# Performance work log

Measured on AMD Instinct MI355X. Metric: run time of the kernel, lower is better.

## Reference

```python
import jax, jax.numpy as jnp
import numpy as np

GATE_DIM = 1313 + 622  # hardcoded in the module
D1 = 300
D2 = 300
OUT = 300


def setup_inputs() -> dict:
    key = jax.random.key(0)
    ks = jax.random.split(key, 12)
    N, M = 384, 384
    inp = {
        "feature1": jax.random.normal(ks[0], (N, GATE_DIM), jnp.float32),
        "box1": jax.random.uniform(ks[1], (N, 5), jnp.float32),
        "feature2": jax.random.normal(ks[2], (M, GATE_DIM), jnp.float32),
        "box2": jax.random.uniform(ks[3], (M, 5), jnp.float32),
        "attrlabel_embeddings": jax.random.normal(ks[4], (GATE_DIM, D1), jnp.float32) * 0.05,
        # learned parameters
        "gate1": 10.0 * jnp.ones((GATE_DIM,), jnp.float32),
        "gate2": 10.0 * jnp.ones((GATE_DIM,), jnp.float32),
        "weight_loc": jnp.zeros((2,), jnp.float32),
        "fc1_w": jax.random.normal(ks[5], (OUT, D1 + D2), jnp.float32) * (1.0 / np.sqrt(D1 + D2)),
        "fc1_b": jnp.zeros((OUT,), jnp.float32),
        "fc2_w": jax.random.normal(ks[6], (OUT, 10), jnp.float32) * (1.0 / np.sqrt(10.0)),
        "fc2_b": jnp.zeros((OUT,), jnp.float32),
        "fc3_w": jax.random.normal(ks[7], (OUT, OUT), jnp.float32) * (1.0 / np.sqrt(OUT)),
        "fc3_b": jnp.zeros((OUT,), jnp.float32),
    }
    return inp


def _preprocess(feature, box):
    # repo's preprocess callable; modeled as identity on the feature
    # (feature already has dim input_dim1/input_dim2 expected by fc1)
    return feature


def reference(feature1, box1, feature2, box2, attrlabel_embeddings,
              gate1, gate2, weight_loc,
              fc1_w, fc1_b, fc2_w, fc2_b, fc3_w, fc3_b):
    # gated feature -> attrlabel embedding projection
    f1 = (feature1 * jax.nn.sigmoid(gate1)) @ attrlabel_embeddings  # [N, D1]
    f1 = _preprocess(f1, box1)
    f2 = (feature2 * jax.nn.sigmoid(gate2)) @ attrlabel_embeddings  # [M, D2]
    f2 = _preprocess(f2, box2)

    # fc1(cat(meshgrid(f1,f2))) == f1@W_a^T (broadcast over M) + f2@W_b^T (broadcast over N) + b
    Wa, Wb = fc1_w[:, :f1.shape[-1]], fc1_w[:, f1.shape[-1]:]
    semantic = jax.nn.relu(
        jnp.einsum('nd,od->no', f1, Wa)[:, None, :]
        + jnp.einsum('md,od->mo', f2, Wb)[None, :, :]
        + fc1_b
    )  # [N, M, OUT]

    Wa2, Wb2 = fc2_w[:, :5], fc2_w[:, 5:]
    spatial = jax.nn.relu(
        jnp.einsum('nd,od->no', box1, Wa2)[:, None, :]
        + jnp.einsum('md,od->mo', box2, Wb2)[None, :, :]
        + fc2_b
    )  # [N, M, OUT]

    w = jax.nn.softmax(weight_loc)
    mixed = w[0] * semantic + w[1] * spatial
    embedding = jnp.einsum('nmo,po->nmp', mixed, fc3_w) + fc3_b  # [N, M, OUT]
    return embedding
```

## Files before the change

kernel.cpp:

```cpp
#include <hip/hip_runtime.h>
#include <hip/hip_bf16.h>

#define NROW 384
#define GD   1935
#define GK   1952
#define DD   300
#define KP   320
#define DP   304

#define OFF_SIG1 0
#define OFF_SIG2 2048
#define OFF_W    4096
#define OFF_XBF  4112
#define OFF_EBT  753680
#define OFF_FC1B 1066000
#define OFF_FC3B 1168400
#define OFF_F1B  1217040
#define OFF_AB   1339920
#define OFF_CD   1585680

typedef short short8 __attribute__((ext_vector_type(8)));
typedef float floatx4 __attribute__((ext_vector_type(4)));

__device__ inline unsigned short f2bf(float x){
  union { float f; unsigned u; } v; v.f = x;
  unsigned r = v.u + 0x7fffu + ((v.u >> 16) & 1u);
  return (unsigned short)(r >> 16);
}

__global__ void k_prep(const float* g1, const float* g2, const float* wloc, float* ws){
  int t = blockIdx.x * 256 + threadIdx.x;
  if (t < GD) ws[OFF_SIG1 + t] = 1.f / (1.f + expf(-g1[t]));
  else if (t < 2*GD) ws[OFF_SIG2 + t - GD] = 1.f / (1.f + expf(-g2[t - GD]));
  else if (t == 2*GD){
    float a = wloc[0], b = wloc[1];
    float m = fmaxf(a, b);
    float ea = expf(a - m), eb = expf(b - m);
    ws[OFF_W + 0] = ea / (ea + eb);
    ws[OFF_W + 1] = eb / (ea + eb);
  }
}

#define NX  (2*384*GK)
#define NE  (KP*GK)
#define NF1 (2*KP*KP)
#define NF3 (DP*KP)
__global__ void k_cvt_all(const float* f1, const float* f2, const float* E,
                          const float* fc1w, const float* fc3w, float* ws){
  int t = blockIdx.x * 256 + threadIdx.x;
  unsigned short* xbf  = (unsigned short*)(ws + OFF_XBF);
  unsigned short* ebt  = (unsigned short*)(ws + OFF_EBT);
  unsigned short* f1b  = (unsigned short*)(ws + OFF_FC1B);
  unsigned short* f3b  = (unsigned short*)(ws + OFF_FC3B);
  if (t < NX){
    int z = t / (384*GK); int r = t - z*384*GK;
    int n = r / GK, k = r - n*GK;
    const float* X   = z ? f2 : f1;
    const float* sig = ws + (z ? OFF_SIG2 : OFF_SIG1);
    float v = (k < GD) ? X[n*GD + k] * sig[k] : 0.f;
    xbf[t] = f2bf(v);
  } else if (t < NX + NE){
    int r = t - NX;
    int c = r / GK, k = r - c*GK;
    float v = (k < GD && c < DD) ? E[k*DD + c] : 0.f;
    ebt[r] = f2bf(v);
  } else if (t < NX + NE + NF1){
    int r = t - NX - NE;
    int z = r / (KP*KP); int r2 = r - z*KP*KP;
    int o = r2 / KP, d = r2 - o*KP;
    float v = (o < DD && d < DD) ? fc1w[o*(2*DD) + z*DD + d] : 0.f;
    f1b[r] = f2bf(v);
  } else {
    int r = t - NX - NE - NF1;
    int p = r / KP, k = r - p*KP;
    float v = (p < DD && k < DD) ? fc3w[p*DD + k] : 0.f;
    f3b[r] = f2bf(v);
  }
}

__global__ __launch_bounds__(256) void k_gg(float* ws){
  int z = blockIdx.y;
  const unsigned short* X   = (const unsigned short*)(ws + OFF_XBF) + z*384*GK;
  const unsigned short* Ebt = (const unsigned short*)(ws + OFF_EBT);
  unsigned short* out       = (unsigned short*)(ws + OFF_F1B) + z*384*KP;
  int t = threadIdx.x, lane = t & 63;
  int id = blockIdx.x * 4 + (t >> 6);
  int mt = id / 20, ct = id - mt*20;
  int col = lane & 15, quad = lane >> 4;
  const unsigned short* ap = X   + (mt*16 + col)*GK + quad*8;
  const unsigned short* bp = Ebt + (ct*16 + col)*GK + quad*8;
  floatx4 acc = (floatx4){0.f,0.f,0.f,0.f};
  for (int kc = 0; kc < 61; ++kc){
    short8 a = *(const short8*)(ap + kc*32);
    short8 b = *(const short8*)(bp + kc*32);
    acc = __builtin_amdgcn_mfma_f32_16x16x32_bf16(a, b, acc, 0, 0, 0);
  }
  int c = ct*16 + col;
  #pragma unroll
  for (int r = 0; r < 4; ++r){
    int m = mt*16 + quad*4 + r;
    out[m*KP + c] = (c < DD) ? f2bf(acc[r]) : (unsigned short)0;
  }
}

__global__ __launch_bounds__(256) void k_sem(const float* fc1b, float* ws){
  int z = blockIdx.y;
  const unsigned short* F = (const unsigned short*)(ws + OFF_F1B) + z*384*KP;
  const unsigned short* W = (const unsigned short*)(ws + OFF_FC1B) + z*KP*KP;
  float* out = ws + OFF_AB + z*384*KP;
  float w0 = ws[OFF_W];
  int t = threadIdx.x, lane = t & 63;
  int id = blockIdx.x * 4 + (t >> 6);
  int rt = id / 20, ot = id - rt*20;
  int col = lane & 15, quad = lane >> 4;
  const unsigned short* ap = F + (rt*16 + col)*KP + quad*8;
  const unsigned short* bp = W + (ot*16 + col)*KP + quad*8;
  floatx4 acc = (floatx4){0.f,0.f,0.f,0.f};
  #pragma unroll
  for (int kc = 0; kc < 10; ++kc){
    short8 a = *(const short8*)(ap + kc*32);
    short8 b = *(const short8*)(bp + kc*32);
    acc = __builtin_amdgcn_mfma_f32_16x16x32_bf16(a, b, acc, 0, 0, 0);
  }
  int o = ot*16 + col;
  float bias = (z == 0 && o < DD) ? fc1b[o] : 0.f;
  #pragma unroll
  for (int r = 0; r < 4; ++r){
    int rr = rt*16 + quad*4 + r;
    out[rr*KP + o] = (o < DD) ? w0 * (acc[r] + bias) : 0.f;
  }
}

__global__ void k_spa(const float* box1, const float* box2, const float* fc2w,
                      const float* fc2b, float* ws){
  int z = blockIdx.y;
  const float* bx = z ? box2 : box1;
  float* out = ws + OFF_CD + z*384*KP;
  int joff = z ? 5 : 0;
  float w1 = ws[OFF_W + 1];
  int t = blockIdx.x * 256 + threadIdx.x;
  int r = t / KP, o = t - r*KP;
  float v = 0.f;
  if (o < DD){
    const float* b = bx + r * 5;
    const float* wr = fc2w + o * 10 + joff;
    v = b[0]*wr[0] + b[1]*wr[1] + b[2]*wr[2] + b[3]*wr[3] + b[4]*wr[4];
    if (!z) v += fc2b[o];
    v *= w1;
  }
  out[t] = v;
}

__global__ __launch_bounds__(512, 4) void k_main(const float* fc3b, float* out, const float* ws){
  __shared__ __align__(16) unsigned short smix[512 * 8];
  __shared__ __align__(16) unsigned short swt[1216 * 8];
  const unsigned short* fc3bf = (const unsigned short*)(ws + OFF_FC3B);
  int t = threadIdx.x;
  int lane = t & 63, wave = t >> 6;
  int col = lane & 15, quad = lane >> 4;
  int mt0 = blockIdx.x * 128;
  int n = blockIdx.y;
  const float* Ah = ws + OFF_AB + n * KP;
  const float* Bh = ws + OFF_AB + 384 * KP;
  const float* Ch = ws + OFF_CD + n * KP;
  const float* Dh = ws + OFF_CD + 384 * KP;

  floatx4 acc[19];
  #pragma unroll
  for (int i = 0; i < 19; ++i) acc[i] = (floatx4){0.f,0.f,0.f,0.f};

  int w_b  = t >> 6;
  int j    = (t >> 4) & 3;
  int colb = t & 15;
  int mg = mt0 + w_b*16 + colb;
  const float* pB = Bh + (size_t)mg * KP;
  const float* pD = Dh + (size_t)mg * KP;

  for (int kc = 0; kc < 10; ++kc){
    int kb = kc*32 + j*8;
    {
      union { unsigned short s[8]; uint4 v; } u;
      float4 a0 = *(const float4*)(Ah + kb);
      float4 c0 = *(const float4*)(Ch + kb);
      float4 b0 = *(const float4*)(pB + kb);
      float4 d0 = *(const float4*)(pD + kb);
      u.s[0] = f2bf(fmaxf(a0.x + b0.x, 0.f) + fmaxf(c0.x + d0.x, 0.f));
      u.s[1] = f2bf(fmaxf(a0.y + b0.y, 0.f) + fmaxf(c0.y + d0.y, 0.f));
      u.s[2] = f2bf(fmaxf(a0.z + b0.z, 0.f) + fmaxf(c0.z + d0.z, 0.f));
      u.s[3] = f2bf(fmaxf(a0.w + b0.w, 0.f) + fmaxf(c0.w + d0.w, 0.f));
      float4 a1 = *(const float4*)(Ah + kb + 4);
      float4 c1 = *(const float4*)(Ch + kb + 4);
      float4 b1 = *(const float4*)(pB + kb + 4);
      float4 d1 = *(const float4*)(pD + kb + 4);
      u.s[4] = f2bf(fmaxf(a1.x + b1.x, 0.f) + fmaxf(c1.x + d1.x, 0.f));
      u.s[5] = f2bf(fmaxf(a1.y + b1.y, 0.f) + fmaxf(c1.y + d1.y, 0.f));
      u.s[6] = f2bf(fmaxf(a1.z + b1.z, 0.f) + fmaxf(c1.z + d1.z, 0.f));
      u.s[7] = f2bf(fmaxf(a1.w + b1.w, 0.f) + fmaxf(c1.w + d1.w, 0.f));
      *(uint4*)&smix[t * 8] = u.v;
    }
    for (int s = t; s < 1216; s += 512){
      int pt = s >> 6, l = s & 63;
      int cc = l & 15, qq = l >> 4;
      uint4 w = *(const uint4*)(fc3bf + (pt*16 + cc)*KP + kc*32 + qq*8);
      *(uint4*)&swt[s * 8] = w;
    }
    __syncthreads();
    short8 af = *(const short8*)&smix[(wave*64 + lane) * 8];
    #pragma unroll
    for (int pt = 0; pt < 19; ++pt){
      short8 bf = *(const short8*)&swt[(pt*64 + lane) * 8];
      acc[pt] = __builtin_amdgcn_mfma_f32_16x16x32_bf16(af, bf, acc[pt], 0, 0, 0);
    }
    __syncthreads();
  }

  #pragma unroll
  for (int pt = 0; pt < 19; ++pt){
    int p = pt*16 + col;
    if (p < DD){
      float bias = fc3b[p];
      #pragma unroll
      for (int r = 0; r < 4; ++r){
        int m = mt0 + wave*16 + quad*4 + r;
        out[((size_t)n * NROW + m) * DD + p] = acc[pt][r] + bias;
      }
    }
  }
}

extern "C" void kernel_launch(void* const* d_in, const int* in_sizes, int n_in,
                              void* d_out, int out_size, void* d_ws, size_t ws_size,
                              hipStream_t stream) {
  const float* feature1 = (const float*)d_in[0];
  const float* box1     = (const float*)d_in[1];
  const float* feature2 = (const float*)d_in[2];
  const float* box2     = (const float*)d_in[3];
  const float* E        = (const float*)d_in[4];
  const float* gate1    = (const float*)d_in[5];
  const float* gate2    = (const float*)d_in[6];
  const float* wloc     = (const float*)d_in[7];
  const float* fc1w     = (const float*)d_in[8];
  const float* fc1b     = (const float*)d_in[9];
  const float* fc2w     = (const float*)d_in[10];
  const float* fc2b     = (const float*)d_in[11];
  const float* fc3w     = (const float*)d_in[12];
  const float* fc3b     = (const float*)d_in[13];
  float* out = (float*)d_out;
  float* ws  = (float*)d_ws;

  hipLaunchKernelGGL(k_prep, dim3(16), dim3(256), 0, stream, gate1, gate2, wloc, ws);
  hipLaunchKernelGGL(k_cvt_all, dim3((NX+NE+NF1+NF3)/256), dim3(256), 0, stream,
                     feature1, feature2, E, fc1w, fc3w, ws);
  hipLaunchKernelGGL(k_gg, dim3(120, 2), dim3(256), 0, stream, ws);
  hipLaunchKernelGGL(k_sem, dim3(120, 2), dim3(256), 0, stream, fc1b, ws);
  hipLaunchKernelGGL(k_spa, dim3(480, 2), dim3(256), 0, stream,
                     box1, box2, fc2w, fc2b, ws);
  hipLaunchKernelGGL(k_main, dim3(3, NROW), dim3(512), 0, stream, fc3b, out, ws);
}
```

Before: 335.7 us.

## Drop LDS staging in main GEMM; load MFMA fragments directly from global

The main fused mix+fc3 kernel no longer stages the mixed activations and fc3 weights through shared memory with two barriers per k-chunk. Each wave now computes its own A fragment in registers and reads the B fragments for all 19 output tiles straight from global memory (L2/L1-resident bf16 weights). Block size drops from 512 to 256 threads and the grid doubles. This removes the LDS traffic and synchronisation, but every wave now issues its own global weight loads, with far less reuse per block and more cache pressure.

```diff
diff --git a/kernel.cpp b/kernel.cpp
--- a/kernel.cpp
+++ b/kernel.cpp
@@ -151,67 +151,53 @@
   out[t] = v;
 }
 
-__global__ __launch_bounds__(512, 4) void k_main(const float* fc3b, float* out, const float* ws){
-  __shared__ __align__(16) unsigned short smix[512 * 8];
-  __shared__ __align__(16) unsigned short swt[1216 * 8];
+__global__ __launch_bounds__(256, 3) void k_main(const float* fc3b, float* out, const float* ws){
   const unsigned short* fc3bf = (const unsigned short*)(ws + OFF_FC3B);
   int t = threadIdx.x;
   int lane = t & 63, wave = t >> 6;
   int col = lane & 15, quad = lane >> 4;
-  int mt0 = blockIdx.x * 128;
   int n = blockIdx.y;
+  int mrow0 = blockIdx.x * 64 + wave * 16;
   const float* Ah = ws + OFF_AB + n * KP;
   const float* Bh = ws + OFF_AB + 384 * KP;
   const float* Ch = ws + OFF_CD + n * KP;
   const float* Dh = ws + OFF_CD + 384 * KP;
 
-  floatx4 acc[19];
-  #pragma unroll
-  for (int i = 0; i < 19; ++i) acc[i] = (floatx4){0.f,0.f,0.f,0.f};
-
-  int w_b  = t >> 6;
-  int j    = (t >> 4) & 3;
-  int colb = t & 15;
-  int mg = mt0 + w_b*16 + colb;
+  int mg = mrow0 + col;
   const float* pB = Bh + (size_t)mg * KP;
   const float* pD = Dh + (size_t)mg * KP;
+  const unsigned short* wbase = fc3bf + col * KP + quad * 8;
+
+  floatx4 acc[19];
+  #pragma unroll
+  for (int i = 0; i < 19; ++i) acc[i] = (floatx4){0.f,0.f,0.f,0.f};
 
   for (int kc = 0; kc < 10; ++kc){
-    int kb = kc*32 + j*8;
-    {
-      union { unsigned short s[8]; uint4 v; } u;
-      float4 a0 = *(const float4*)(Ah + kb);
-      float4 c0 = *(const float4*)(Ch + kb);
-      float4 b0 = *(const float4*)(pB + kb);
-      float4 d0 = *(const float4*)(pD + kb);
-      u.s[0] = f2bf(fmaxf(a0.x + b0.x, 0.f) + fmaxf(c0.x + d0.x, 0.f));
-      u.s[1] = f2bf(fmaxf(a0.y + b0.y, 0.f) + fmaxf(c0.y + d0.y, 0.f));
-      u.s[2] = f2bf(fmaxf(a0.z + b0.z, 0.f) + fmaxf(c0.z + d0.z, 0.f));
-      u.s[3] = f2bf(fmaxf(a0.w + b0.w, 0.f) + fmaxf(c0.w + d0.w, 0.f));
-      float4 a1 = *(const float4*)(Ah + kb + 4);
-      float4 c1 = *(const float4*)(Ch + kb + 4);
-      float4 b1 = *(const float4*)(pB + kb + 4);
-      float4 d1 = *(const float4*)(pD + kb + 4);
-      u.s[4] = f2bf(fmaxf(a1.x + b1.x, 0.f) + fmaxf(c1.x + d1.x, 0.f));
-      u.s[5] = f2bf(fmaxf(a1.y + b1.y, 0.f) + fmaxf(c1.y + d1.y, 0.f));
-      u.s[6] = f2bf(fmaxf(a1.z + b1.z, 0.f) + fmaxf(c1.z + d1.z, 0.f));
-      u.s[7] = f2bf(fmaxf(a1.w + b1.w, 0.f) + fmaxf(c1.w + d1.w, 0.f));
-      *(uint4*)&smix[t * 8] = u.v;
-    }
-    for (int s = t; s < 1216; s += 512){
-      int pt = s >> 6, l = s & 63;
-      int cc = l & 15, qq = l >> 4;
-      uint4 w = *(const uint4*)(fc3bf + (pt*16 + cc)*KP + kc*32 + qq*8);
-      *(uint4*)&swt[s * 8] = w;
-    }
-    __syncthreads();
-    short8 af = *(const short8*)&smix[(wave*64 + lane) * 8];
+    int kb = kc*32 + quad*8;
+    union { unsigned short s[8]; short8 v8; } u;
+    float4 a0 = *(const float4*)(Ah + kb);
+    float4 c0 = *(const float4*)(Ch + kb);
+    float4 b0 = *(const float4*)(pB + kb);
+    float4 d0 = *(const float4*)(pD + kb);
+    u.s[0] = f2bf(fmaxf(a0.x + b0.x, 0.f) + fmaxf(c0.x + d0.x, 0.f));
+    u.s[1] = f2bf(fmaxf(a0.y + b0.y, 0.f) + fmaxf(c0.y + d0.y, 0.f));
+    u.s[2] = f2bf(fmaxf(a0.z + b0.z, 0.f) + fmaxf(c0.z + d0.z, 0.f));
+    u.s[3] = f2bf(fmaxf(a0.w + b0.w, 0.f) + fmaxf(c0.w + d0.w, 0.f));
+    float4 a1 = *(const float4*)(Ah + kb + 4);
+    float4 c1 = *(const float4*)(Ch + kb + 4);
+    float4 b1 = *(const float4*)(pB + kb + 4);
+    float4 d1 = *(const float4*)(pD + kb + 4);
+    u.s[4] = f2bf(fmaxf(a1.x + b1.x, 0.f) + fmaxf(c1.x + d1.x, 0.f));
+    u.s[5] = f2bf(fmaxf(a1.y + b1.y, 0.f) + fmaxf(c1.y + d1.y, 0.f));
+    u.s[6] = f2bf(fmaxf(a1.z + b1.z, 0.f) + fmaxf(c1.z + d1.z, 0.f));
+    u.s[7] = f2bf(fmaxf(a1.w + b1.w, 0.f) + fmaxf(c1.w + d1.w, 0.f));
+    short8 af = u.v8;
+    const unsigned short* wk = wbase + kc*32;
     #pragma unroll
     for (int pt = 0; pt < 19; ++pt){
-      short8 bf = *(const short8*)&swt[(pt*64 + lane) * 8];
+      short8 bf = *(const short8*)(wk + pt*16*KP);
       acc[pt] = __builtin_amdgcn_mfma_f32_16x16x32_bf16(af, bf, acc[pt], 0, 0, 0);
     }
-    __syncthreads();
   }
 
   #pragma unroll
@@ -221,7 +207,7 @@
       float bias = fc3b[p];
       #pragma unroll
       for (int r = 0; r < 4; ++r){
-        int m = mt0 + wave*16 + quad*4 + r;
+        int m = mrow0 + quad*4 + r;
         out[((size_t)n * NROW + m) * DD + p] = acc[pt][r] + bias;
       }
     }
@@ -255,5 +241,5 @@
   hipLaunchKernelGGL(k_sem, dim3(120, 2), dim3(256), 0, stream, fc1b, ws);
   hipLaunchKernelGGL(k_spa, dim3(480, 2), dim3(256), 0, stream,
                      box1, box2, fc2w, fc2b, ws);
-  hipLaunchKernelGGL(k_main, dim3(3, NROW), dim3(512), 0, stream, fc3b, out, ws);
-}
+  hipLaunchKernelGGL(k_main, dim3(6, NROW), dim3(256), 0, stream, fc3b, out, ws);
+}
```

Measured after the change: 542.8 us. 1.62x slower.
